# Kernel optimization log

Hardware: AMD Instinct MI355X
Metric: run time of the kernel (lower is better)

Reference implementation:

```python
import jax, jax.numpy as jnp
import numpy as np

B, T, I, U, BB = 256, 1024, 64, 128, 256


def lecun_tanh(x):
    return 1.7159 * jnp.tanh(0.666 * x)


def _linear_init(key, fan_in, fan_out):
    # torch nn.Linear default: U(-1/sqrt(fan_in), 1/sqrt(fan_in)) for weight and bias
    kw, kb = jax.random.split(key)
    lim = 1.0 / np.sqrt(fan_in)
    W = jax.random.uniform(kw, (fan_in, fan_out), jnp.float32, -lim, lim)
    b = jax.random.uniform(kb, (fan_out,), jnp.float32, -lim, lim)
    return W, b


def setup_inputs() -> dict:
    key = jax.random.key(0)
    ks = jax.random.split(key, 6)
    x = jax.random.normal(ks[0], (B, T, I), jnp.float32)
    W_bb, b_bb = _linear_init(ks[1], I + U, BB)
    W_ff1, b_ff1 = _linear_init(ks[2], BB, U)
    W_ff2, b_ff2 = _linear_init(ks[3], BB, U)
    W_ta, b_ta = _linear_init(ks[4], BB, U)
    W_tb, b_tb = _linear_init(ks[5], BB, U)
    return {
        "x": x,
        "W_bb": W_bb, "b_bb": b_bb,
        "W_ff1": W_ff1, "b_ff1": b_ff1,
        "W_ff2": W_ff2, "b_ff2": b_ff2,
        "W_ta": W_ta, "b_ta": b_ta,
        "W_tb": W_tb, "b_tb": b_tb,
    }


def reference(x, W_bb, b_bb, W_ff1, b_ff1, W_ff2, b_ff2, W_ta, b_ta, W_tb, b_tb):
    # CfC, non-wired, mode='default', activation='lecun_tanh', backbone_layers=1,
    # mixed_memory=False, proj_size=None (fc = Identity), timespans=None (ts = 1.0).
    ts = jnp.float32(1.0)

    def step(h, xt):
        z = jnp.concatenate([xt, h], axis=-1)            # [B, I+U]
        z = lecun_tanh(z @ W_bb + b_bb)                   # backbone, [B, BB]
        ff1 = jnp.tanh(z @ W_ff1 + b_ff1)                 # [B, U]
        ff2 = jnp.tanh(z @ W_ff2 + b_ff2)                 # [B, U]
        t_a = z @ W_ta + b_ta
        t_b = z @ W_tb + b_tb
        t_interp = jax.nn.sigmoid(t_a * ts + t_b)
        h_new = ff1 * (1.0 - t_interp) + t_interp * ff2
        return h_new, h_new

    h0 = jnp.zeros((x.shape[0], W_ff1.shape[1]), x.dtype)
    h_last, ys = jax.lax.scan(step, h0, jnp.swapaxes(x, 0, 1))  # scan over T
    readout = jnp.swapaxes(ys, 0, 1)                      # [B, T, U]
    return readout, h_last
```

## Files before the change

### kernel.cpp

```cpp
#include <hip/hip_runtime.h>


typedef __bf16 bf16;
typedef __bf16 bf16x8 __attribute__((ext_vector_type(8)));
typedef float  f32x4  __attribute__((ext_vector_type(4)));

#define BDIM 512

constexpr int B_  = 256;
constexpr int T_  = 1024;
constexpr int I_  = 64;
constexpr int U_  = 128;
constexpr int BB_ = 256;
constexpr int ROWS = 16;
constexpr int NBLK = B_ / ROWS;
constexpr int KO1  = (I_ + U_) / 8;

__device__ __forceinline__ float tanh_fast(float x) {
  float e = __builtin_amdgcn_exp2f(x * 2.8853900817779268f);
  return 1.0f - 2.0f * __builtin_amdgcn_rcpf(e + 1.0f);
}
__device__ __forceinline__ float sigmoid_fast(float x) {
  return __builtin_amdgcn_rcpf(1.0f + __builtin_amdgcn_exp2f(x * -1.4426950408889634f));
}

__device__ __forceinline__ void barrier_lds() {
  asm volatile("s_waitcnt lgkmcnt(0)" ::: "memory");
  __builtin_amdgcn_s_barrier();
}

__global__ __launch_bounds__(512, 2)
void xz_precompute(const float* __restrict__ x,
                   const float* __restrict__ Wbb,
                   const float* __restrict__ bbb,
                   float4* __restrict__ ws)
{
  const int tid  = threadIdx.x;
  const int w    = tid >> 6;
  const int l    = tid & 63;
  const int quad = l >> 4;
  const int l16  = l & 15;
  const int bg   = blockIdx.x >> 4;
  const int t0   = (blockIdx.x & 15) * 64;

  const int c1 = w * 32 + l16;

  bf16x8 fx[2][2];
  #pragma unroll
  for (int ks = 0; ks < 2; ks++)
    #pragma unroll
    for (int nt = 0; nt < 2; nt++)
      #pragma unroll
      for (int j = 0; j < 8; j++)
        fx[ks][nt][j] = (bf16)Wbb[(ks * 32 + quad * 8 + j) * BB_ + c1 + nt * 16];

  const float bz0 = bbb[c1];
  const float bz1 = bbb[c1 + 16];

  const float* xs = x + ((size_t)(bg * ROWS + l16) * T_) * I_ + quad * 8;

  for (int t = t0; t < t0 + 64; ++t) {
    const float* xt = xs + (size_t)t * I_;
    float4 a0lo = *(const float4*)(xt);
    float4 a0hi = *(const float4*)(xt + 4);
    float4 a1lo = *(const float4*)(xt + 32);
    float4 a1hi = *(const float4*)(xt + 36);

    bf16x8 af[2];
    af[0][0]=(bf16)a0lo.x; af[0][1]=(bf16)a0lo.y; af[0][2]=(bf16)a0lo.z; af[0][3]=(bf16)a0lo.w;
    af[0][4]=(bf16)a0hi.x; af[0][5]=(bf16)a0hi.y; af[0][6]=(bf16)a0hi.z; af[0][7]=(bf16)a0hi.w;
    af[1][0]=(bf16)a1lo.x; af[1][1]=(bf16)a1lo.y; af[1][2]=(bf16)a1lo.z; af[1][3]=(bf16)a1lo.w;
    af[1][4]=(bf16)a1hi.x; af[1][5]=(bf16)a1hi.y; af[1][6]=(bf16)a1hi.z; af[1][7]=(bf16)a1hi.w;

    f32x4 az0 = { bz0, bz0, bz0, bz0 };
    f32x4 az1 = { bz1, bz1, bz1, bz1 };
    #pragma unroll
    for (int ks = 0; ks < 2; ks++) {
      az0 = __builtin_amdgcn_mfma_f32_16x16x32_bf16(af[ks], fx[ks][0], az0, 0, 0, 0);
      az1 = __builtin_amdgcn_mfma_f32_16x16x32_bf16(af[ks], fx[ks][1], az1, 0, 0, 0);
    }
    size_t base = ((size_t)((bg * T_ + t) * 8 + w) * 2) * 64 + l;
    ws[base]      = *(const float4*)&az0;
    ws[base + 64] = *(const float4*)&az1;
  }
}

__global__ __launch_bounds__(BDIM, 2)
void cfc_kernel_ws(const float* __restrict__ Wbb,
                   const float* __restrict__ Wff1, const float* __restrict__ bff1,
                   const float* __restrict__ Wff2, const float* __restrict__ bff2,
                   const float* __restrict__ Wta,  const float* __restrict__ bta,
                   const float* __restrict__ Wtb,  const float* __restrict__ btb,
                   const float4* __restrict__ ws,
                   float* __restrict__ out)
{
  __shared__ __align__(16) bf16 Abuf[16 * ROWS * 8];
  __shared__ __align__(16) bf16 Zbuf[32 * ROWS * 8];

  const int tid  = threadIdx.x;
  const int w    = tid >> 6;
  const int l    = tid & 63;
  const int quad = l >> 4;
  const int l16  = l & 15;
  const int bg   = blockIdx.x;

  const int c1 = w * 32 + l16;
  const int u  = w * 16 + l16;

  bf16x8 f1h[4][2];
  #pragma unroll
  for (int ks = 0; ks < 4; ks++)
    #pragma unroll
    for (int nt = 0; nt < 2; nt++)
      #pragma unroll
      for (int j = 0; j < 8; j++) {
        int k = 64 + ks * 32 + quad * 8 + j;
        f1h[ks][nt][j] = (bf16)Wbb[k * BB_ + c1 + nt * 16];
      }

  bf16x8 g2[8][3];
  #pragma unroll
  for (int r = 0; r < 8; r++) {
    int ks = (w + r) & 7;
    #pragma unroll
    for (int j = 0; j < 8; j++) {
      int k = ks * 32 + quad * 8 + j;
      g2[r][0][j] = (bf16)Wff1[k * U_ + u];
      g2[r][1][j] = (bf16)Wff2[k * U_ + u];
      g2[r][2][j] = (bf16)(Wta[k * U_ + u] + Wtb[k * U_ + u]);
    }
  }

  const float bh0 = bff1[u];
  const float bh1 = bff2[u];
  const float bh2 = bta[u] + btb[u];

  for (int idx = tid; idx < 16 * ROWS * 8; idx += BDIM)
    Abuf[idx] = (bf16)0.0f;
  __syncthreads();

  float* outp  = out + (size_t)(bg * ROWS) * T_ * U_ + u;
  float* hlast = out + (size_t)B_ * T_ * U_ + (size_t)(bg * ROWS) * U_ + u;

  const int h_oct = u >> 3;
  const int h_sub = u & 7;

  float hreg[4];

  const float4* wsp = ws + ((size_t)(bg * T_) * 8 + w) * 2 * 64 + l;
  float4 xz0 = wsp[0];
  float4 xz1 = wsp[64];

  for (int t = 0; t < T_; ++t) {
    if (t) {
      #pragma unroll
      for (int i = 0; i < 4; i++)
        outp[(size_t)(quad * 4 + i) * T_ * U_ + (size_t)(t - 1) * U_] = hreg[i];
    }

    f32x4 az0 = *(const f32x4*)&xz0;
    f32x4 az1 = *(const f32x4*)&xz1;
    #pragma unroll
    for (int ks = 0; ks < 4; ks++) {
      bf16x8 a = *(const bf16x8*)&Abuf[((ks * 4 + quad) * ROWS + l16) * 8];
      az0 = __builtin_amdgcn_mfma_f32_16x16x32_bf16(a, f1h[ks][0], az0, 0, 0, 0);
      az1 = __builtin_amdgcn_mfma_f32_16x16x32_bf16(a, f1h[ks][1], az1, 0, 0, 0);
    }
    #pragma unroll
    for (int i = 0; i < 4; i++) {
      int m = quad * 4 + i;
      float z0 = 1.7159f * tanh_fast(0.666f * az0[i]);
      float z1 = 1.7159f * tanh_fast(0.666f * az1[i]);
      int c0 = c1, cB = c1 + 16;
      Zbuf[((c0 >> 3) * ROWS + m) * 8 + (c0 & 7)] = (bf16)z0;
      Zbuf[((cB >> 3) * ROWS + m) * 8 + (cB & 7)] = (bf16)z1;
    }

    f32x4 a0 = { bh0, bh0, bh0, bh0 };
    f32x4 a1 = { bh1, bh1, bh1, bh1 };
    f32x4 a2 = { bh2, bh2, bh2, bh2 };
    {
      bf16x8 zf0 = *(const bf16x8*)&Zbuf[((w * 4 + quad) * ROWS + l16) * 8];
      a0 = __builtin_amdgcn_mfma_f32_16x16x32_bf16(zf0, g2[0][0], a0, 0, 0, 0);
      a1 = __builtin_amdgcn_mfma_f32_16x16x32_bf16(zf0, g2[0][1], a1, 0, 0, 0);
      a2 = __builtin_amdgcn_mfma_f32_16x16x32_bf16(zf0, g2[0][2], a2, 0, 0, 0);
    }
    barrier_lds();

    bf16x8 zf[7];
    #pragma unroll
    for (int r = 1; r < 8; r++) {
      const int ks = (w + r) & 7;
      zf[r - 1] = *(const bf16x8*)&Zbuf[((ks * 4 + quad) * ROWS + l16) * 8];
    }

    {
      const int tn = (t + 1 < T_) ? (t + 1) : (T_ - 1);
      const float4* p = wsp + (size_t)tn * (8 * 2 * 64);
      xz0 = p[0];
      xz1 = p[64];
    }

    #pragma unroll
    for (int r = 1; r < 8; r++) {
      a0 = __builtin_amdgcn_mfma_f32_16x16x32_bf16(zf[r - 1], g2[r][0], a0, 0, 0, 0);
      a1 = __builtin_amdgcn_mfma_f32_16x16x32_bf16(zf[r - 1], g2[r][1], a1, 0, 0, 0);
    }
    #pragma unroll
    for (int r = 1; r < 8; r++)
      a2 = __builtin_amdgcn_mfma_f32_16x16x32_bf16(zf[r - 1], g2[r][2], a2, 0, 0, 0);

    float ff1v[4], ff2v[4];
    #pragma unroll
    for (int i = 0; i < 4; i++) ff1v[i] = tanh_fast(a0[i]);
    #pragma unroll
    for (int i = 0; i < 4; i++) ff2v[i] = tanh_fast(a1[i]);

    #pragma unroll
    for (int i = 0; i < 4; i++) {
      int m = quad * 4 + i;
      float s = sigmoid_fast(a2[i]);
      float h = ff1v[i] + s * (ff2v[i] - ff1v[i]);
      hreg[i] = h;
      Abuf[(h_oct * ROWS + m) * 8 + h_sub] = (bf16)h;
    }

    barrier_lds();
  }

  #pragma unroll
  for (int i = 0; i < 4; i++) {
    outp[(size_t)(quad * 4 + i) * T_ * U_ + (size_t)(T_ - 1) * U_] = hreg[i];
    hlast[(size_t)(quad * 4 + i) * U_] = hreg[i];
  }
}

__global__ __launch_bounds__(BDIM, 2)
void cfc_kernel_fb(const float* __restrict__ x,
                   const float* __restrict__ Wbb,  const float* __restrict__ bbb,
                   const float* __restrict__ Wff1, const float* __restrict__ bff1,
                   const float* __restrict__ Wff2, const float* __restrict__ bff2,
                   const float* __restrict__ Wta,  const float* __restrict__ bta,
                   const float* __restrict__ Wtb,  const float* __restrict__ btb,
                   float* __restrict__ out)
{
  __shared__ __align__(16) bf16 Abuf[KO1 * ROWS * 8];
  __shared__ __align__(16) bf16 Zbuf[32  * ROWS * 8];

  const int tid  = threadIdx.x;
  const int w    = tid >> 6;
  const int l    = tid & 63;
  const int quad = l >> 4;
  const int l16  = l & 15;
  const int bg   = blockIdx.x;

  const int c1 = w * 32 + l16;
  const int u  = w * 16 + l16;

  bf16x8 f1[6][2];
  #pragma unroll
  for (int ks = 0; ks < 6; ks++)
    #pragma unroll
    for (int nt = 0; nt < 2; nt++)
      #pragma unroll
      for (int j = 0; j < 8; j++) {
        int k = ks * 32 + quad * 8 + j;
        f1[ks][nt][j] = (bf16)Wbb[k * BB_ + c1 + nt * 16];
      }

  bf16x8 g2[8][3];
  #pragma unroll
  for (int r = 0; r < 8; r++) {
    int ks = (w + r) & 7;
    #pragma unroll
    for (int j = 0; j < 8; j++) {
      int k = ks * 32 + quad * 8 + j;
      g2[r][0][j] = (bf16)Wff1[k * U_ + u];
      g2[r][1][j] = (bf16)Wff2[k * U_ + u];
      g2[r][2][j] = (bf16)(Wta[k * U_ + u] + Wtb[k * U_ + u]);
    }
  }

  const float bz0 = bbb[c1];
  const float bz1 = bbb[c1 + 16];
  const float bh0 = bff1[u];
  const float bh1 = bff2[u];
  const float bh2 = bta[u] + btb[u];

  for (int idx = tid; idx < (KO1 - 8) * ROWS * 8; idx += BDIM)
    Abuf[8 * ROWS * 8 + idx] = (bf16)0.0f;

  const int xm  = tid >> 5;
  const int xkk = tid & 31;
  const float* xsrc = x + ((size_t)(bg * ROWS + xm) * T_) * I_ + 2 * xkk;
  bf16* xdst = &Abuf[(((2 * xkk) >> 3) * ROWS + xm) * 8 + ((2 * xkk) & 7)];

  {
    float2 v = *(const float2*)xsrc;
    xdst[0] = (bf16)v.x;
    xdst[1] = (bf16)v.y;
  }
  __syncthreads();

  float* outp  = out + (size_t)(bg * ROWS) * T_ * U_ + u;
  float* hlast = out + (size_t)B_ * T_ * U_ + (size_t)(bg * ROWS) * U_ + u;

  const int h_oct = (64 + u) >> 3;
  const int h_sub = (64 + u) & 7;

  float hreg[4];
  float2 xv_cur = *(const float2*)(xsrc + I_);

  for (int t = 0; t < T_; ++t) {
    if (t) {
      #pragma unroll
      for (int i = 0; i < 4; i++)
        outp[(size_t)(quad * 4 + i) * T_ * U_ + (size_t)(t - 1) * U_] = hreg[i];
    }

    f32x4 az0 = { bz0, bz0, bz0, bz0 };
    f32x4 az1 = { bz1, bz1, bz1, bz1 };
    #pragma unroll
    for (int ks = 0; ks < 6; ks++) {
      bf16x8 a = *(const bf16x8*)&Abuf[((ks * 4 + quad) * ROWS + l16) * 8];
      az0 = __builtin_amdgcn_mfma_f32_16x16x32_bf16(a, f1[ks][0], az0, 0, 0, 0);
      az1 = __builtin_amdgcn_mfma_f32_16x16x32_bf16(a, f1[ks][1], az1, 0, 0, 0);
    }
    #pragma unroll
    for (int i = 0; i < 4; i++) {
      int m = quad * 4 + i;
      float z0 = 1.7159f * tanh_fast(0.666f * az0[i]);
      float z1 = 1.7159f * tanh_fast(0.666f * az1[i]);
      int c0 = c1, cB = c1 + 16;
      Zbuf[((c0 >> 3) * ROWS + m) * 8 + (c0 & 7)] = (bf16)z0;
      Zbuf[((cB >> 3) * ROWS + m) * 8 + (cB & 7)] = (bf16)z1;
    }

    f32x4 a0 = { bh0, bh0, bh0, bh0 };
    f32x4 a1 = { bh1, bh1, bh1, bh1 };
    f32x4 a2 = { bh2, bh2, bh2, bh2 };
    {
      bf16x8 zf0 = *(const bf16x8*)&Zbuf[((w * 4 + quad) * ROWS + l16) * 8];
      a0 = __builtin_amdgcn_mfma_f32_16x16x32_bf16(zf0, g2[0][0], a0, 0, 0, 0);
      a1 = __builtin_amdgcn_mfma_f32_16x16x32_bf16(zf0, g2[0][1], a1, 0, 0, 0);
      a2 = __builtin_amdgcn_mfma_f32_16x16x32_bf16(zf0, g2[0][2], a2, 0, 0, 0);
    }
    barrier_lds();

    bf16x8 zf[7];
    #pragma unroll
    for (int r = 1; r < 8; r++) {
      const int ks = (w + r) & 7;
      zf[r - 1] = *(const bf16x8*)&Zbuf[((ks * 4 + quad) * ROWS + l16) * 8];
    }

    xdst[0] = (bf16)xv_cur.x;
    xdst[1] = (bf16)xv_cur.y;
    {
      const int tn = (t + 2 < T_) ? (t + 2) : (T_ - 1);
      xv_cur = *(const float2*)(xsrc + (size_t)tn * I_);
    }

    #pragma unroll
    for (int r = 1; r < 8; r++) {
      a0 = __builtin_amdgcn_mfma_f32_16x16x32_bf16(zf[r - 1], g2[r][0], a0, 0, 0, 0);
      a1 = __builtin_amdgcn_mfma_f32_16x16x32_bf16(zf[r - 1], g2[r][1], a1, 0, 0, 0);
    }
    #pragma unroll
    for (int r = 1; r < 8; r++)
      a2 = __builtin_amdgcn_mfma_f32_16x16x32_bf16(zf[r - 1], g2[r][2], a2, 0, 0, 0);

    float ff1v[4], ff2v[4];
    #pragma unroll
    for (int i = 0; i < 4; i++) ff1v[i] = tanh_fast(a0[i]);
    #pragma unroll
    for (int i = 0; i < 4; i++) ff2v[i] = tanh_fast(a1[i]);

    #pragma unroll
    for (int i = 0; i < 4; i++) {
      int m = quad * 4 + i;
      float s = sigmoid_fast(a2[i]);
      float h = ff1v[i] + s * (ff2v[i] - ff1v[i]);
      hreg[i] = h;
      Abuf[(h_oct * ROWS + m) * 8 + h_sub] = (bf16)h;
    }

    barrier_lds();
  }

  #pragma unroll
  for (int i = 0; i < 4; i++) {
    outp[(size_t)(quad * 4 + i) * T_ * U_ + (size_t)(T_ - 1) * U_] = hreg[i];
    hlast[(size_t)(quad * 4 + i) * U_] = hreg[i];
  }
}

extern "C" void kernel_launch(void* const* d_in, const int* in_sizes, int n_in,
                              void* d_out, int out_size, void* d_ws, size_t ws_size,
                              hipStream_t stream) {
  const float* x    = (const float*)d_in[0];
  const float* Wbb  = (const float*)d_in[1];
  const float* bbb  = (const float*)d_in[2];
  const float* Wff1 = (const float*)d_in[3];
  const float* bff1 = (const float*)d_in[4];
  const float* Wff2 = (const float*)d_in[5];
  const float* bff2 = (const float*)d_in[6];
  const float* Wta  = (const float*)d_in[7];
  const float* bta  = (const float*)d_in[8];
  const float* Wtb  = (const float*)d_in[9];
  const float* btb  = (const float*)d_in[10];
  float* out = (float*)d_out;
  (void)in_sizes; (void)n_in; (void)out_size;

  const size_t need = (size_t)NBLK * T_ * 8 * 2 * 64 * sizeof(float4);

  if (d_ws != nullptr && ws_size >= need) {
    float4* ws = (float4*)d_ws;
    hipLaunchKernelGGL(xz_precompute, dim3(256), dim3(512), 0, stream,
                       x, Wbb, bbb, ws);
    hipLaunchKernelGGL(cfc_kernel_ws, dim3(NBLK), dim3(BDIM), 0, stream,
                       Wbb, Wff1, bff1, Wff2, bff2, Wta, bta, Wtb, btb,
                       (const float4*)ws, out);
  } else {
    hipLaunchKernelGGL(cfc_kernel_fb, dim3(NBLK), dim3(BDIM), 0, stream,
                       x, Wbb, bbb, Wff1, bff1, Wff2, bff2, Wta, bta, Wtb, btb, out);
  }
}
```

Measured before the change: 1.548 ms.

## Specialize waves into backbone and head groups in the recurrent kernel

Splits the eight waves of each block into two roles. Waves 0-3 compute the backbone pre-activation and lecun_tanh into the z buffer, with four column tiles per wave. Waves 4-7 compute the ff1/ff2/time-gate heads and the new hidden state, with two unit tiles per wave. The aim is to shrink each wave's resident weight-fragment set and specialize its work. Because the backbone and head stages depend strictly on each other every step, only half the waves are busy in each phase and each wave's serial MFMA chain doubles, which can lengthen the per-step critical path.

Result: slower. 2.642 ms (+70.6%).

```diff
diff --git a/kernel.cpp b/kernel.cpp
--- a/kernel.cpp
+++ b/kernel.cpp
@@ -79,7 +79,7 @@
       az0 = __builtin_amdgcn_mfma_f32_16x16x32_bf16(af[ks], fx[ks][0], az0, 0, 0, 0);
       az1 = __builtin_amdgcn_mfma_f32_16x16x32_bf16(af[ks], fx[ks][1], az1, 0, 0, 0);
     }
-    size_t base = ((size_t)((bg * T_ + t) * 8 + w) * 2) * 64 + l;
+    size_t base = ((size_t)(bg * T_ + t) * 16 + w * 2) * 64 + l;
     ws[base]      = *(const float4*)&az0;
     ws[base + 64] = *(const float4*)&az1;
   }
@@ -104,134 +104,147 @@
   const int l16  = l & 15;
   const int bg   = blockIdx.x;
 
-  const int c1 = w * 32 + l16;
-  const int u  = w * 16 + l16;
-
-  bf16x8 f1h[4][2];
-  #pragma unroll
-  for (int ks = 0; ks < 4; ks++)
-    #pragma unroll
-    for (int nt = 0; nt < 2; nt++)
-      #pragma unroll
-      for (int j = 0; j < 8; j++) {
-        int k = 64 + ks * 32 + quad * 8 + j;
-        f1h[ks][nt][j] = (bf16)Wbb[k * BB_ + c1 + nt * 16];
-      }
-
-  bf16x8 g2[8][3];
-  #pragma unroll
-  for (int r = 0; r < 8; r++) {
-    int ks = (w + r) & 7;
-    #pragma unroll
-    for (int j = 0; j < 8; j++) {
-      int k = ks * 32 + quad * 8 + j;
-      g2[r][0][j] = (bf16)Wff1[k * U_ + u];
-      g2[r][1][j] = (bf16)Wff2[k * U_ + u];
-      g2[r][2][j] = (bf16)(Wta[k * U_ + u] + Wtb[k * U_ + u]);
-    }
-  }
-
-  const float bh0 = bff1[u];
-  const float bh1 = bff2[u];
-  const float bh2 = bta[u] + btb[u];
-
   for (int idx = tid; idx < 16 * ROWS * 8; idx += BDIM)
     Abuf[idx] = (bf16)0.0f;
   __syncthreads();
 
-  float* outp  = out + (size_t)(bg * ROWS) * T_ * U_ + u;
-  float* hlast = out + (size_t)B_ * T_ * U_ + (size_t)(bg * ROWS) * U_ + u;
-
-  const int h_oct = u >> 3;
-  const int h_sub = u & 7;
-
-  float hreg[4];
-
-  const float4* wsp = ws + ((size_t)(bg * T_) * 8 + w) * 2 * 64 + l;
-  float4 xz0 = wsp[0];
-  float4 xz1 = wsp[64];
-
-  for (int t = 0; t < T_; ++t) {
-    if (t) {
-      #pragma unroll
-      for (int i = 0; i < 4; i++)
-        outp[(size_t)(quad * 4 + i) * T_ * U_ + (size_t)(t - 1) * U_] = hreg[i];
-    }
-
-    f32x4 az0 = *(const f32x4*)&xz0;
-    f32x4 az1 = *(const f32x4*)&xz1;
-    #pragma unroll
-    for (int ks = 0; ks < 4; ks++) {
-      bf16x8 a = *(const bf16x8*)&Abuf[((ks * 4 + quad) * ROWS + l16) * 8];
-      az0 = __builtin_amdgcn_mfma_f32_16x16x32_bf16(a, f1h[ks][0], az0, 0, 0, 0);
-      az1 = __builtin_amdgcn_mfma_f32_16x16x32_bf16(a, f1h[ks][1], az1, 0, 0, 0);
-    }
-    #pragma unroll
-    for (int i = 0; i < 4; i++) {
-      int m = quad * 4 + i;
-      float z0 = 1.7159f * tanh_fast(0.666f * az0[i]);
-      float z1 = 1.7159f * tanh_fast(0.666f * az1[i]);
-      int c0 = c1, cB = c1 + 16;
-      Zbuf[((c0 >> 3) * ROWS + m) * 8 + (c0 & 7)] = (bf16)z0;
-      Zbuf[((cB >> 3) * ROWS + m) * 8 + (cB & 7)] = (bf16)z1;
-    }
-
-    f32x4 a0 = { bh0, bh0, bh0, bh0 };
-    f32x4 a1 = { bh1, bh1, bh1, bh1 };
-    f32x4 a2 = { bh2, bh2, bh2, bh2 };
-    {
-      bf16x8 zf0 = *(const bf16x8*)&Zbuf[((w * 4 + quad) * ROWS + l16) * 8];
-      a0 = __builtin_amdgcn_mfma_f32_16x16x32_bf16(zf0, g2[0][0], a0, 0, 0, 0);
-      a1 = __builtin_amdgcn_mfma_f32_16x16x32_bf16(zf0, g2[0][1], a1, 0, 0, 0);
-      a2 = __builtin_amdgcn_mfma_f32_16x16x32_bf16(zf0, g2[0][2], a2, 0, 0, 0);
-    }
-    barrier_lds();
-
-    bf16x8 zf[7];
-    #pragma unroll
-    for (int r = 1; r < 8; r++) {
-      const int ks = (w + r) & 7;
-      zf[r - 1] = *(const bf16x8*)&Zbuf[((ks * 4 + quad) * ROWS + l16) * 8];
-    }
-
-    {
-      const int tn = (t + 1 < T_) ? (t + 1) : (T_ - 1);
-      const float4* p = wsp + (size_t)tn * (8 * 2 * 64);
-      xz0 = p[0];
-      xz1 = p[64];
-    }
-
-    #pragma unroll
-    for (int r = 1; r < 8; r++) {
-      a0 = __builtin_amdgcn_mfma_f32_16x16x32_bf16(zf[r - 1], g2[r][0], a0, 0, 0, 0);
-      a1 = __builtin_amdgcn_mfma_f32_16x16x32_bf16(zf[r - 1], g2[r][1], a1, 0, 0, 0);
-    }
-    #pragma unroll
-    for (int r = 1; r < 8; r++)
-      a2 = __builtin_amdgcn_mfma_f32_16x16x32_bf16(zf[r - 1], g2[r][2], a2, 0, 0, 0);
-
-    float ff1v[4], ff2v[4];
-    #pragma unroll
-    for (int i = 0; i < 4; i++) ff1v[i] = tanh_fast(a0[i]);
-    #pragma unroll
-    for (int i = 0; i < 4; i++) ff2v[i] = tanh_fast(a1[i]);
-
-    #pragma unroll
-    for (int i = 0; i < 4; i++) {
-      int m = quad * 4 + i;
-      float s = sigmoid_fast(a2[i]);
-      float h = ff1v[i] + s * (ff2v[i] - ff1v[i]);
-      hreg[i] = h;
-      Abuf[(h_oct * ROWS + m) * 8 + h_sub] = (bf16)h;
-    }
-
-    barrier_lds();
-  }
-
-  #pragma unroll
-  for (int i = 0; i < 4; i++) {
-    outp[(size_t)(quad * 4 + i) * T_ * U_ + (size_t)(T_ - 1) * U_] = hreg[i];
-    hlast[(size_t)(quad * 4 + i) * U_] = hreg[i];
+  if (w < 4) {
+    bf16x8 f1h[4][4];
+    #pragma unroll
+    for (int ks = 0; ks < 4; ks++)
+      #pragma unroll
+      for (int nt = 0; nt < 4; nt++)
+        #pragma unroll
+        for (int j = 0; j < 8; j++) {
+          int k = 64 + ks * 32 + quad * 8 + j;
+          f1h[ks][nt][j] = (bf16)Wbb[k * BB_ + w * 64 + nt * 16 + l16];
+        }
+
+    const float4* wsp = ws + ((size_t)bg * T_ * 16 + w * 4) * 64 + l;
+    float4 xz[4];
+    #pragma unroll
+    for (int nt = 0; nt < 4; nt++) xz[nt] = wsp[nt * 64];
+
+    for (int t = 0; t < T_; ++t) {
+      f32x4 az[4];
+      #pragma unroll
+      for (int nt = 0; nt < 4; nt++) az[nt] = *(const f32x4*)&xz[nt];
+      #pragma unroll
+      for (int ks = 0; ks < 4; ks++) {
+        bf16x8 a = *(const bf16x8*)&Abuf[((ks * 4 + quad) * ROWS + l16) * 8];
+        #pragma unroll
+        for (int nt = 0; nt < 4; nt++)
+          az[nt] = __builtin_amdgcn_mfma_f32_16x16x32_bf16(a, f1h[ks][nt], az[nt], 0, 0, 0);
+      }
+      #pragma unroll
+      for (int nt = 0; nt < 4; nt++) {
+        const int c = w * 64 + nt * 16 + l16;
+        #pragma unroll
+        for (int i = 0; i < 4; i++) {
+          int m = quad * 4 + i;
+          float zv = 1.7159f * tanh_fast(0.666f * az[nt][i]);
+          Zbuf[((c >> 3) * ROWS + m) * 8 + (c & 7)] = (bf16)zv;
+        }
+      }
+      barrier_lds();
+
+      {
+        const int tn = (t + 1 < T_) ? (t + 1) : (T_ - 1);
+        const float4* p = wsp + (size_t)tn * (16 * 64);
+        #pragma unroll
+        for (int nt = 0; nt < 4; nt++) xz[nt] = p[nt * 64];
+      }
+      barrier_lds();
+    }
+  } else {
+    const int w4 = w - 4;
+    const int u0 = w4 * 32 + l16;
+
+    bf16x8 g2[8][2][3];
+    #pragma unroll
+    for (int r = 0; r < 8; r++) {
+      int ks = (2 * w4 + r) & 7;
+      #pragma unroll
+      for (int nt = 0; nt < 2; nt++)
+        #pragma unroll
+        for (int j = 0; j < 8; j++) {
+          int k = ks * 32 + quad * 8 + j;
+          int u = u0 + nt * 16;
+          g2[r][nt][0][j] = (bf16)Wff1[k * U_ + u];
+          g2[r][nt][1][j] = (bf16)Wff2[k * U_ + u];
+          g2[r][nt][2][j] = (bf16)(Wta[k * U_ + u] + Wtb[k * U_ + u]);
+        }
+    }
+
+    float bh[2][3];
+    #pragma unroll
+    for (int nt = 0; nt < 2; nt++) {
+      bh[nt][0] = bff1[u0 + nt * 16];
+      bh[nt][1] = bff2[u0 + nt * 16];
+      bh[nt][2] = bta[u0 + nt * 16] + btb[u0 + nt * 16];
+    }
+
+    float* outp  = out + (size_t)(bg * ROWS) * T_ * U_ + u0;
+    float* hlast = out + (size_t)B_ * T_ * U_ + (size_t)(bg * ROWS) * U_ + u0;
+    const int h_oct = u0 >> 3;
+    const int h_sub = u0 & 7;
+
+    float hreg[2][4];
+
+    for (int t = 0; t < T_; ++t) {
+      if (t) {
+        #pragma unroll
+        for (int nt = 0; nt < 2; nt++)
+          #pragma unroll
+          for (int i = 0; i < 4; i++)
+            outp[(size_t)(quad * 4 + i) * T_ * U_ + (size_t)(t - 1) * U_ + nt * 16] = hreg[nt][i];
+      }
+      barrier_lds();
+
+      f32x4 acc[2][3];
+      #pragma unroll
+      for (int nt = 0; nt < 2; nt++)
+        #pragma unroll
+        for (int o = 0; o < 3; o++)
+          acc[nt][o] = f32x4{ bh[nt][o], bh[nt][o], bh[nt][o], bh[nt][o] };
+
+      #pragma unroll
+      for (int r = 0; r < 8; r++) {
+        const int ks = (2 * w4 + r) & 7;
+        bf16x8 zf = *(const bf16x8*)&Zbuf[((ks * 4 + quad) * ROWS + l16) * 8];
+        #pragma unroll
+        for (int nt = 0; nt < 2; nt++)
+          #pragma unroll
+          for (int o = 0; o < 3; o++)
+            acc[nt][o] = __builtin_amdgcn_mfma_f32_16x16x32_bf16(zf, g2[r][nt][o], acc[nt][o], 0, 0, 0);
+      }
+
+      #pragma unroll
+      for (int nt = 0; nt < 2; nt++) {
+        float ff1v[4], ff2v[4];
+        #pragma unroll
+        for (int i = 0; i < 4; i++) ff1v[i] = tanh_fast(acc[nt][0][i]);
+        #pragma unroll
+        for (int i = 0; i < 4; i++) ff2v[i] = tanh_fast(acc[nt][1][i]);
+        #pragma unroll
+        for (int i = 0; i < 4; i++) {
+          int m = quad * 4 + i;
+          float s = sigmoid_fast(acc[nt][2][i]);
+          float h = ff1v[i] + s * (ff2v[i] - ff1v[i]);
+          hreg[nt][i] = h;
+          Abuf[((h_oct + nt * 2) * ROWS + m) * 8 + h_sub] = (bf16)h;
+        }
+      }
+      barrier_lds();
+    }
+
+    #pragma unroll
+    for (int nt = 0; nt < 2; nt++)
+      #pragma unroll
+      for (int i = 0; i < 4; i++) {
+        outp[(size_t)(quad * 4 + i) * T_ * U_ + (size_t)(T_ - 1) * U_ + nt * 16] = hreg[nt][i];
+        hlast[(size_t)(quad * 4 + i) * U_ + nt * 16] = hreg[nt][i];
+      }
   }
 }
 
@@ -412,7 +425,7 @@
   float* out = (float*)d_out;
   (void)in_sizes; (void)n_in; (void)out_size;
 
-  const size_t need = (size_t)NBLK * T_ * 8 * 2 * 64 * sizeof(float4);
+  const size_t need = (size_t)NBLK * T_ * 16 * 64 * sizeof(float4);
 
   if (d_ws != nullptr && ws_size >= need) {
     float4* ws = (float4*)d_ws;
```
